# Performance work log

Hardware: AMD Instinct MI355X
Metric: run time of the kernel (lower is better)

## Reference

```python
import jax, jax.numpy as jnp
import numpy as np
from jax.ops import segment_sum


def gcn_conv(x, edge_index, W, b):
    """PyG GCNConv: add self-loops, symmetric D^-1/2 (A+I) D^-1/2 normalization,
    then aggregate normalized messages at target nodes. edge_weight=None -> ones."""
    N = x.shape[0]
    loops = jnp.arange(N, dtype=edge_index.dtype)
    row = jnp.concatenate([edge_index[0], loops])  # source nodes
    col = jnp.concatenate([edge_index[1], loops])  # target nodes
    w = jnp.ones(row.shape[0], dtype=x.dtype)
    deg = segment_sum(w, col, num_segments=N)
    dinv = jnp.where(deg > 0, jax.lax.rsqrt(deg), 0.0)
    norm = dinv[row] * dinv[col]                    # [E+N]
    xw = x @ W                                      # dense transform [N, out]
    msg = xw[row] * norm[:, None]                   # gather + scale [E+N, out]
    out = segment_sum(msg, col, num_segments=N)     # scatter-add at targets
    return out + b


def setup_inputs() -> dict:
    key = jax.random.key(0)
    k1, k2, k3, k4 = jax.random.split(key, 4)
    N, E, nhid, nfeat = 50000, 800000, 256, 128
    x = jax.random.normal(k1, (N, nhid), dtype=jnp.float32)
    edge_index = jax.random.randint(k2, (2, E), 0, N, dtype=jnp.int64)
    W1 = jax.random.normal(k3, (nhid, nhid), dtype=jnp.float32) * (1.0 / np.sqrt(nhid))
    b1 = jnp.zeros((nhid,), dtype=jnp.float32)
    W2 = jax.random.normal(k4, (nhid, nfeat), dtype=jnp.float32) * (1.0 / np.sqrt(nhid))
    b2 = jnp.zeros((nfeat,), dtype=jnp.float32)
    return {"x": x, "edge_index": edge_index, "W1": W1, "b1": b1, "W2": W2, "b2": b2}


def reference(x, edge_index, W1, b1, W2, b2):
    h = jax.nn.relu(gcn_conv(x, edge_index, W1, b1))
    # dropout is identity in eval mode (deterministic reference)
    return gcn_conv(h, edge_index, W2, b2)
```

## Files before the change

### kernel.cpp

```cpp
#include <hip/hip_runtime.h>
#include <math.h>


typedef _Float16 h8 __attribute__((ext_vector_type(8)));
typedef float    f32x4 __attribute__((ext_vector_type(4)));

__global__ void k_init(int* __restrict__ deg, int N,
                       const float* __restrict__ W1, const float* __restrict__ W2,
                       _Float16* __restrict__ wt1, _Float16* __restrict__ wt2,
                       int K, int n1, int n2, int zb)
{
    if ((int)blockIdx.x < zb) {
        int i = blockIdx.x * blockDim.x + threadIdx.x;
        if (i < N) deg[i] = 0;
    } else {
        int i = (blockIdx.x - zb) * blockDim.x + threadIdx.x;
        int c1 = K * n1;
        if (i < c1) {
            int k = i / n1, n = i % n1;
            wt1[(long)n * K + k] = (_Float16)W1[i];
        } else if (i < c1 + K * n2) {
            int j = i - c1;
            int k = j / n2, n = j % n2;
            wt2[(long)n * K + k] = (_Float16)W2[j];
        }
    }
}

__global__ void k_count(const int* __restrict__ col, int E,
                        int* __restrict__ deg, int* __restrict__ rank) {
    int i = blockIdx.x * blockDim.x + threadIdx.x;
    int s = gridDim.x * blockDim.x;
    for (int e = i; e < E; e += s) rank[e] = atomicAdd(&deg[col[e]], 1);
}

__global__ __launch_bounds__(1024) void k_scan1(const int* __restrict__ deg, int N,
                                                int* __restrict__ incl, int* __restrict__ bsum) {
    __shared__ int sm[1024];
    int t = threadIdx.x;
    int i = blockIdx.x * 1024 + t;
    sm[t] = (i < N) ? deg[i] : 0;
    __syncthreads();
    for (int off = 1; off < 1024; off <<= 1) {
        int add = (t >= off) ? sm[t - off] : 0;
        __syncthreads();
        sm[t] += add;
        __syncthreads();
    }
    incl[i] = sm[t];
    if (t == 1023) bsum[blockIdx.x] = sm[t];
}

__global__ void k_scan2(const int* __restrict__ bsum, int* __restrict__ boff, int nb) {
    if (threadIdx.x == 0 && blockIdx.x == 0) {
        int run = 0;
        for (int b = 0; b < nb; b++) { boff[b] = run; run += bsum[b]; }
    }
}

__global__ void k_scan3(const int* __restrict__ incl, const int* __restrict__ boff,
                        const int* __restrict__ deg, int N,
                        int* __restrict__ rowptr, float* __restrict__ dinv) {
    int i = blockIdx.x * blockDim.x + threadIdx.x;
    if (i < N) {
        rowptr[i + 1] = incl[i] + boff[i >> 10];
        dinv[i] = rsqrtf((float)(1 + deg[i]));
    }
    if (i == 0) rowptr[0] = 0;
}

template<bool A32>
__device__ __forceinline__ void gemm_body(
    const float* __restrict__ X32, const _Float16* __restrict__ X16,
    const _Float16* __restrict__ Wt, const float* __restrict__ dinv,
    _Float16* __restrict__ Y, int M, int K, int NC, int bx, int by)
{
    __shared__ _Float16 As[128][40];
    __shared__ _Float16 Bs[128][40];

    const int bn = bx * 128;
    const int bm = by * 128;
    const int tid = threadIdx.x;
    const int w = tid >> 6, l = tid & 63;
    const int wm = (w >> 1) * 64, wn = (w & 1) * 64;
    const int lr = l & 15, lg = l >> 4;

    f32x4 acc[4][4];
    #pragma unroll
    for (int i = 0; i < 4; i++)
        #pragma unroll
        for (int j = 0; j < 4; j++)
            acc[i][j] = (f32x4){0.f, 0.f, 0.f, 0.f};

    for (int k0 = 0; k0 < K; k0 += 32) {
        if (A32) {
            #pragma unroll
            for (int p = 0; p < 2; p++) {
                int rowi = p * 64 + (tid >> 2);
                int colA = (tid & 3) * 8;
                int gm = bm + rowi; if (gm >= M) gm = M - 1;
                float4 f0 = *reinterpret_cast<const float4*>(&X32[(long)gm * K + k0 + colA]);
                float4 f1 = *reinterpret_cast<const float4*>(&X32[(long)gm * K + k0 + colA + 4]);
                h8 hv;
                hv[0] = (_Float16)f0.x; hv[1] = (_Float16)f0.y;
                hv[2] = (_Float16)f0.z; hv[3] = (_Float16)f0.w;
                hv[4] = (_Float16)f1.x; hv[5] = (_Float16)f1.y;
                hv[6] = (_Float16)f1.z; hv[7] = (_Float16)f1.w;
                *reinterpret_cast<h8*>(&As[rowi][colA]) = hv;
            }
        } else {
            int rowi = tid >> 1;
            int colA = (tid & 1) * 16;
            int gm = bm + rowi; if (gm >= M) gm = M - 1;
            *reinterpret_cast<h8*>(&As[rowi][colA]) =
                *reinterpret_cast<const h8*>(&X16[(long)gm * K + k0 + colA]);
            *reinterpret_cast<h8*>(&As[rowi][colA + 8]) =
                *reinterpret_cast<const h8*>(&X16[(long)gm * K + k0 + colA + 8]);
        }
        {
            int n = tid >> 1;
            int colB = (tid & 1) * 16;
            *reinterpret_cast<h8*>(&Bs[n][colB]) =
                *reinterpret_cast<const h8*>(&Wt[(long)(bn + n) * K + k0 + colB]);
            *reinterpret_cast<h8*>(&Bs[n][colB + 8]) =
                *reinterpret_cast<const h8*>(&Wt[(long)(bn + n) * K + k0 + colB + 8]);
        }
        __syncthreads();

        h8 a[4], b[4];
        #pragma unroll
        for (int i = 0; i < 4; i++)
            a[i] = *reinterpret_cast<const h8*>(&As[wm + i * 16 + lr][lg * 8]);
        #pragma unroll
        for (int j = 0; j < 4; j++)
            b[j] = *reinterpret_cast<const h8*>(&Bs[wn + j * 16 + lr][lg * 8]);
        #pragma unroll
        for (int i = 0; i < 4; i++)
            #pragma unroll
            for (int j = 0; j < 4; j++)
                acc[i][j] = __builtin_amdgcn_mfma_f32_16x16x32_f16(
                    a[i], b[j], acc[i][j], 0, 0, 0);
        __syncthreads();
    }

    #pragma unroll
    for (int i = 0; i < 4; i++) {
        #pragma unroll
        for (int r = 0; r < 4; r++) {
            int gm = bm + wm + i * 16 + lg * 4 + r;
            if (gm < M) {
                float s = dinv[gm];
                #pragma unroll
                for (int j = 0; j < 4; j++)
                    Y[(long)gm * NC + bn + wn + j * 16 + lr] =
                        (_Float16)(acc[i][j][r] * s);
            }
        }
    }
}

__global__ __launch_bounds__(256) void k_fill_gemm(
    const int* __restrict__ row, const int* __restrict__ col,
    const int* __restrict__ rank, int E,
    const int* __restrict__ rowptr, int* __restrict__ srcidx,
    int nfb,
    const float* __restrict__ X32, const _Float16* __restrict__ Wt,
    const float* __restrict__ dinv, _Float16* __restrict__ Y,
    int M, int K, int NC, int gx)
{
    if ((int)blockIdx.x < nfb) {
        int i = blockIdx.x * blockDim.x + threadIdx.x;
        int s = nfb * blockDim.x;
        for (int e = i; e < E; e += s) {
            int c = col[e];
            srcidx[rowptr[c] + rank[e]] = row[e];
        }
        return;
    }
    int gb = blockIdx.x - nfb;
    gemm_body<true>(X32, nullptr, Wt, dinv, Y, M, K, NC, gb % gx, gb / gx);
}

__global__ __launch_bounds__(256) void k_gemm16(
    const _Float16* __restrict__ X16, const _Float16* __restrict__ Wt,
    const float* __restrict__ dinv, _Float16* __restrict__ Y,
    int M, int K, int NC)
{
    gemm_body<false>(nullptr, X16, Wt, dinv, Y, M, K, NC, blockIdx.x, blockIdx.y);
}

template<int LPR, bool F16OUT, bool RELU>
__global__ __launch_bounds__(256) void k_agg(
    const int* __restrict__ rowptr, const int* __restrict__ srcidx,
    const _Float16* __restrict__ Y, const float* __restrict__ dinv,
    const float* __restrict__ bias, int N, int FT, int fo,
    float* __restrict__ out32, _Float16* __restrict__ out16)
{
    const int G = 64 / LPR;
    int node = blockIdx.x * 4 + (threadIdx.x >> 6);
    if (node >= N) return;
    int lane = threadIdx.x & 63;
    int sub = lane / LPR;
    int fl  = lane % LPR;
    const int fcol = fo + fl * 8;

    float acc[8];
    if (sub == 0) {
        h8 v = *reinterpret_cast<const h8*>(&Y[(long)node * FT + fcol]);
        #pragma unroll
        for (int j = 0; j < 8; j++) acc[j] = (float)v[j];
    } else {
        #pragma unroll
        for (int j = 0; j < 8; j++) acc[j] = 0.f;
    }

    int beg = rowptr[node], end = rowptr[node + 1];
    int cnt = end - beg;
    int i = beg + sub;
    int full = cnt / (4 * G);
    for (int t = 0; t < full; t++) {
        int r0 = srcidx[i];
        int r1 = srcidx[i + G];
        int r2 = srcidx[i + 2 * G];
        int r3 = srcidx[i + 3 * G];
        h8 v0 = *reinterpret_cast<const h8*>(&Y[(long)r0 * FT + fcol]);
        h8 v1 = *reinterpret_cast<const h8*>(&Y[(long)r1 * FT + fcol]);
        h8 v2 = *reinterpret_cast<const h8*>(&Y[(long)r2 * FT + fcol]);
        h8 v3 = *reinterpret_cast<const h8*>(&Y[(long)r3 * FT + fcol]);
        #pragma unroll
        for (int j = 0; j < 8; j++)
            acc[j] += ((float)v0[j] + (float)v1[j]) + ((float)v2[j] + (float)v3[j]);
        i += 4 * G;
    }
    for (; i < end; i += G) {
        int r = srcidx[i];
        h8 v = *reinterpret_cast<const h8*>(&Y[(long)r * FT + fcol]);
        #pragma unroll
        for (int j = 0; j < 8; j++) acc[j] += (float)v[j];
    }

    #pragma unroll
    for (int m = LPR; m < 64; m <<= 1)
        #pragma unroll
        for (int j = 0; j < 8; j++)
            acc[j] += __shfl_xor(acc[j], m, 64);

    float s = dinv[node];
    const float4* b4 = reinterpret_cast<const float4*>(&bias[fcol]);
    float4 blo = b4[0], bhi = b4[1];
    float r8[8];
    r8[0] = fmaf(s, acc[0], blo.x); r8[1] = fmaf(s, acc[1], blo.y);
    r8[2] = fmaf(s, acc[2], blo.z); r8[3] = fmaf(s, acc[3], blo.w);
    r8[4] = fmaf(s, acc[4], bhi.x); r8[5] = fmaf(s, acc[5], bhi.y);
    r8[6] = fmaf(s, acc[6], bhi.z); r8[7] = fmaf(s, acc[7], bhi.w);
    if (RELU) {
        #pragma unroll
        for (int j = 0; j < 8; j++) r8[j] = fmaxf(r8[j], 0.f);
    }

    long base = (long)node * FT + fcol;
    if (F16OUT) {
        if (sub == 0) {
            h8 o;
            #pragma unroll
            for (int j = 0; j < 8; j++) o[j] = (_Float16)r8[j];
            *reinterpret_cast<h8*>(&out16[base]) = o;
        }
    } else {
        if (sub == 0) {
            *reinterpret_cast<float4*>(&out32[base]) =
                make_float4(r8[0], r8[1], r8[2], r8[3]);
        } else if (sub == 1) {
            *reinterpret_cast<float4*>(&out32[base + 4]) =
                make_float4(r8[4], r8[5], r8[6], r8[7]);
        }
    }
}

extern "C" void kernel_launch(void* const* d_in, const int* in_sizes, int n_in,
                              void* d_out, int out_size, void* d_ws, size_t ws_size,
                              hipStream_t stream)
{
    const float* x   = (const float*)d_in[0];
    const int*   ei  = (const int*)d_in[1];
    const float* W1  = (const float*)d_in[2];
    const float* b1  = (const float*)d_in[3];
    const float* W2  = (const float*)d_in[4];
    const float* b2  = (const float*)d_in[5];

    const int nhid  = in_sizes[3];
    const int nfeat = in_sizes[5];
    const int N     = in_sizes[0] / nhid;
    const int E     = in_sizes[1] / 2;

    const int* row = ei;
    const int* col = ei + E;

    const int nb = (N + 1023) / 1024;

    size_t cur = 0;
    auto alloc = [&](size_t bytes) {
        void* p = (char*)d_ws + cur;
        cur += (bytes + 255) & ~(size_t)255;
        return p;
    };
    float*     dinv   = (float*)alloc((size_t)N * 4);
    int*       deg_i  = (int*)alloc((size_t)N * 4);
    int*       rank   = (int*)alloc((size_t)E * 4);
    int*       rowptr = (int*)alloc((size_t)(N + 1) * 4);
    int*       incl   = (int*)alloc((size_t)nb * 1024 * 4);
    int*       bsum   = (int*)alloc((size_t)nb * 4);
    int*       boff   = (int*)alloc((size_t)nb * 4);
    int*       srcidx = (int*)alloc((size_t)E * 4);
    _Float16*  wt1    = (_Float16*)alloc((size_t)nhid * nhid * 2);
    _Float16*  wt2    = (_Float16*)alloc((size_t)nhid * nfeat * 2);
    _Float16*  y16    = (_Float16*)alloc((size_t)N * nhid * 2);
    _Float16*  h16    = (_Float16*)alloc((size_t)N * nhid * 2);
    _Float16*  y2     = (_Float16*)alloc((size_t)N * nfeat * 2);
    float*     out    = (float*)d_out;
    (void)ws_size; (void)n_in; (void)out_size;

    const int T = 256;

    {
        int zb = (N + T - 1) / T;
        int pb = (nhid * (nhid + nfeat) + T - 1) / T;
        k_init<<<zb + pb, T, 0, stream>>>(deg_i, N, W1, W2, wt1, wt2,
                                          nhid, nhid, nfeat, zb);
    }
    k_count<<<1024, T, 0, stream>>>(col, E, deg_i, rank);
    k_scan1<<<nb, 1024, 0, stream>>>(deg_i, N, incl, bsum);
    k_scan2<<<1, 64, 0, stream>>>(bsum, boff, nb);
    k_scan3<<<(N + T - 1) / T, T, 0, stream>>>(incl, boff, deg_i, N, rowptr, dinv);

    {
        const int nfb = 512;
        int gx = nhid / 128;
        int gy = (N + 127) / 128;
        k_fill_gemm<<<nfb + gx * gy, T, 0, stream>>>(
            row, col, rank, E, rowptr, srcidx, nfb,
            x, wt1, dinv, y16, N, nhid, nhid, gx);
    }

    k_agg<16, true, true><<<(N + 3) / 4, T, 0, stream>>>(
        rowptr, srcidx, y16, dinv, b1, N, nhid, 0, nullptr, h16);
    k_agg<16, true, true><<<(N + 3) / 4, T, 0, stream>>>(
        rowptr, srcidx, y16, dinv, b1, N, nhid, 128, nullptr, h16);

    {
        dim3 grid(nfeat / 128, (N + 127) / 128);
        k_gemm16<<<grid, T, 0, stream>>>(h16, wt2, dinv, y2, N, nhid, nfeat);
    }
    k_agg<16, false, false><<<(N + 3) / 4, T, 0, stream>>>(
        rowptr, srcidx, y2, dinv, b2, N, nfeat, 0, out, nullptr);
}
```

Before: 211.6 us.

## Replace CSR scan with fixed-capacity per-node buckets and overlap counting with GEMM

Drops the three-kernel prefix scan that built rowptr and stores source indices in fixed CAP=64 slots per target node. Edges beyond the cap go to a global overflow list that every aggregation scans. Degree counting now runs alongside the first GEMM, so the GEMM epilogue no longer scales by dinv; the aggregation applies source dinv per edge instead. The GEMM also register-prefetches the next K tile. The cost is a larger srcidx buffer, extra dinv gathers per edge, and a linear overflow scan per node when degrees exceed the cap.

```diff
diff --git a/kernel.cpp b/kernel.cpp
--- a/kernel.cpp
+++ b/kernel.cpp
@@ -5,7 +5,9 @@
 typedef _Float16 h8 __attribute__((ext_vector_type(8)));
 typedef float    f32x4 __attribute__((ext_vector_type(4)));
 
-__global__ void k_init(int* __restrict__ deg, int N,
+#define CAP 64
+
+__global__ void k_init(int* __restrict__ deg, int* __restrict__ govf, int N,
                        const float* __restrict__ W1, const float* __restrict__ W2,
                        _Float16* __restrict__ wt1, _Float16* __restrict__ wt2,
                        int K, int n1, int n2, int zb)
@@ -13,6 +15,7 @@
     if ((int)blockIdx.x < zb) {
         int i = blockIdx.x * blockDim.x + threadIdx.x;
         if (i < N) deg[i] = 0;
+        if (blockIdx.x == 0 && threadIdx.x == 0) *govf = 0;
     } else {
         int i = (blockIdx.x - zb) * blockDim.x + threadIdx.x;
         int c1 = K * n1;
@@ -27,53 +30,11 @@
     }
 }
 
-__global__ void k_count(const int* __restrict__ col, int E,
-                        int* __restrict__ deg, int* __restrict__ rank) {
-    int i = blockIdx.x * blockDim.x + threadIdx.x;
-    int s = gridDim.x * blockDim.x;
-    for (int e = i; e < E; e += s) rank[e] = atomicAdd(&deg[col[e]], 1);
-}
-
-__global__ __launch_bounds__(1024) void k_scan1(const int* __restrict__ deg, int N,
-                                                int* __restrict__ incl, int* __restrict__ bsum) {
-    __shared__ int sm[1024];
-    int t = threadIdx.x;
-    int i = blockIdx.x * 1024 + t;
-    sm[t] = (i < N) ? deg[i] : 0;
-    __syncthreads();
-    for (int off = 1; off < 1024; off <<= 1) {
-        int add = (t >= off) ? sm[t - off] : 0;
-        __syncthreads();
-        sm[t] += add;
-        __syncthreads();
-    }
-    incl[i] = sm[t];
-    if (t == 1023) bsum[blockIdx.x] = sm[t];
-}
-
-__global__ void k_scan2(const int* __restrict__ bsum, int* __restrict__ boff, int nb) {
-    if (threadIdx.x == 0 && blockIdx.x == 0) {
-        int run = 0;
-        for (int b = 0; b < nb; b++) { boff[b] = run; run += bsum[b]; }
-    }
-}
-
-__global__ void k_scan3(const int* __restrict__ incl, const int* __restrict__ boff,
-                        const int* __restrict__ deg, int N,
-                        int* __restrict__ rowptr, float* __restrict__ dinv) {
-    int i = blockIdx.x * blockDim.x + threadIdx.x;
-    if (i < N) {
-        rowptr[i + 1] = incl[i] + boff[i >> 10];
-        dinv[i] = rsqrtf((float)(1 + deg[i]));
-    }
-    if (i == 0) rowptr[0] = 0;
-}
-
 template<bool A32>
 __device__ __forceinline__ void gemm_body(
     const float* __restrict__ X32, const _Float16* __restrict__ X16,
-    const _Float16* __restrict__ Wt, const float* __restrict__ dinv,
-    _Float16* __restrict__ Y, int M, int K, int NC, int bx, int by)
+    const _Float16* __restrict__ Wt, _Float16* __restrict__ Y,
+    int M, int K, int NC, int bx, int by)
 {
     __shared__ _Float16 As[128][40];
     __shared__ _Float16 Bs[128][40];
@@ -85,6 +46,9 @@
     const int wm = (w >> 1) * 64, wn = (w & 1) * 64;
     const int lr = l & 15, lg = l >> 4;
 
+    const int arow = tid >> 2, acol = (tid & 3) * 8;
+    const int xrow = tid >> 1, xcol = (tid & 1) * 16;
+
     f32x4 acc[4][4];
     #pragma unroll
     for (int i = 0; i < 4; i++)
@@ -92,40 +56,52 @@
         for (int j = 0; j < 4; j++)
             acc[i][j] = (f32x4){0.f, 0.f, 0.f, 0.f};
 
+    float4 pf0, pf1, pf2, pf3;
+    h8 pa0, pa1;
+    h8 pb0, pb1;
+
+    auto loadA = [&](int k0) {
+        if (A32) {
+            int gm0 = bm + arow;      if (gm0 >= M) gm0 = M - 1;
+            int gm1 = bm + 64 + arow; if (gm1 >= M) gm1 = M - 1;
+            pf0 = *reinterpret_cast<const float4*>(&X32[(long)gm0 * K + k0 + acol]);
+            pf1 = *reinterpret_cast<const float4*>(&X32[(long)gm0 * K + k0 + acol + 4]);
+            pf2 = *reinterpret_cast<const float4*>(&X32[(long)gm1 * K + k0 + acol]);
+            pf3 = *reinterpret_cast<const float4*>(&X32[(long)gm1 * K + k0 + acol + 4]);
+        } else {
+            int gm = bm + xrow; if (gm >= M) gm = M - 1;
+            pa0 = *reinterpret_cast<const h8*>(&X16[(long)gm * K + k0 + xcol]);
+            pa1 = *reinterpret_cast<const h8*>(&X16[(long)gm * K + k0 + xcol + 8]);
+        }
+    };
+    auto loadB = [&](int k0) {
+        pb0 = *reinterpret_cast<const h8*>(&Wt[(long)(bn + xrow) * K + k0 + xcol]);
+        pb1 = *reinterpret_cast<const h8*>(&Wt[(long)(bn + xrow) * K + k0 + xcol + 8]);
+    };
+
+    loadA(0); loadB(0);
     for (int k0 = 0; k0 < K; k0 += 32) {
         if (A32) {
-            #pragma unroll
-            for (int p = 0; p < 2; p++) {
-                int rowi = p * 64 + (tid >> 2);
-                int colA = (tid & 3) * 8;
-                int gm = bm + rowi; if (gm >= M) gm = M - 1;
-                float4 f0 = *reinterpret_cast<const float4*>(&X32[(long)gm * K + k0 + colA]);
-                float4 f1 = *reinterpret_cast<const float4*>(&X32[(long)gm * K + k0 + colA + 4]);
-                h8 hv;
-                hv[0] = (_Float16)f0.x; hv[1] = (_Float16)f0.y;
-                hv[2] = (_Float16)f0.z; hv[3] = (_Float16)f0.w;
-                hv[4] = (_Float16)f1.x; hv[5] = (_Float16)f1.y;
-                hv[6] = (_Float16)f1.z; hv[7] = (_Float16)f1.w;
-                *reinterpret_cast<h8*>(&As[rowi][colA]) = hv;
-            }
+            h8 h0, h1;
+            h0[0] = (_Float16)pf0.x; h0[1] = (_Float16)pf0.y;
+            h0[2] = (_Float16)pf0.z; h0[3] = (_Float16)pf0.w;
+            h0[4] = (_Float16)pf1.x; h0[5] = (_Float16)pf1.y;
+            h0[6] = (_Float16)pf1.z; h0[7] = (_Float16)pf1.w;
+            h1[0] = (_Float16)pf2.x; h1[1] = (_Float16)pf2.y;
+            h1[2] = (_Float16)pf2.z; h1[3] = (_Float16)pf2.w;
+            h1[4] = (_Float16)pf3.x; h1[5] = (_Float16)pf3.y;
+            h1[6] = (_Float16)pf3.z; h1[7] = (_Float16)pf3.w;
+            *reinterpret_cast<h8*>(&As[arow][acol]) = h0;
+            *reinterpret_cast<h8*>(&As[64 + arow][acol]) = h1;
         } else {
-            int rowi = tid >> 1;
-            int colA = (tid & 1) * 16;
-            int gm = bm + rowi; if (gm >= M) gm = M - 1;
-            *reinterpret_cast<h8*>(&As[rowi][colA]) =
-                *reinterpret_cast<const h8*>(&X16[(long)gm * K + k0 + colA]);
-            *reinterpret_cast<h8*>(&As[rowi][colA + 8]) =
-                *reinterpret_cast<const h8*>(&X16[(long)gm * K + k0 + colA + 8]);
-        }
-        {
-            int n = tid >> 1;
-            int colB = (tid & 1) * 16;
-            *reinterpret_cast<h8*>(&Bs[n][colB]) =
-                *reinterpret_cast<const h8*>(&Wt[(long)(bn + n) * K + k0 + colB]);
-            *reinterpret_cast<h8*>(&Bs[n][colB + 8]) =
-                *reinterpret_cast<const h8*>(&Wt[(long)(bn + n) * K + k0 + colB + 8]);
-        }
+            *reinterpret_cast<h8*>(&As[xrow][xcol]) = pa0;
+            *reinterpret_cast<h8*>(&As[xrow][xcol + 8]) = pa1;
+        }
+        *reinterpret_cast<h8*>(&Bs[xrow][xcol]) = pb0;
+        *reinterpret_cast<h8*>(&Bs[xrow][xcol + 8]) = pb1;
         __syncthreads();
+
+        if (k0 + 32 < K) { loadA(k0 + 32); loadB(k0 + 32); }
 
         h8 a[4], b[4];
         #pragma unroll
@@ -149,51 +125,84 @@
         for (int r = 0; r < 4; r++) {
             int gm = bm + wm + i * 16 + lg * 4 + r;
             if (gm < M) {
-                float s = dinv[gm];
                 #pragma unroll
                 for (int j = 0; j < 4; j++)
                     Y[(long)gm * NC + bn + wn + j * 16 + lr] =
-                        (_Float16)(acc[i][j][r] * s);
+                        (_Float16)acc[i][j][r];
             }
         }
     }
 }
 
-__global__ __launch_bounds__(256) void k_fill_gemm(
+__global__ __launch_bounds__(256) void k_count_gemm(
+    const int* __restrict__ col, int E, int* __restrict__ deg, int* __restrict__ rank,
+    int ncb,
+    const float* __restrict__ X32, const _Float16* __restrict__ Wt,
+    _Float16* __restrict__ Y, int M, int K, int NC, int gx)
+{
+    if ((int)blockIdx.x < ncb) {
+        int i = blockIdx.x * blockDim.x + threadIdx.x;
+        int s = ncb * blockDim.x;
+        for (int e = i; e < E; e += s) rank[e] = atomicAdd(&deg[col[e]], 1);
+        return;
+    }
+    int gb = blockIdx.x - ncb;
+    gemm_body<true>(X32, nullptr, Wt, Y, M, K, NC, gb % gx, gb / gx);
+}
+
+__global__ __launch_bounds__(256) void k_fill_dinv(
     const int* __restrict__ row, const int* __restrict__ col,
     const int* __restrict__ rank, int E,
-    const int* __restrict__ rowptr, int* __restrict__ srcidx,
-    int nfb,
-    const float* __restrict__ X32, const _Float16* __restrict__ Wt,
-    const float* __restrict__ dinv, _Float16* __restrict__ Y,
-    int M, int K, int NC, int gx)
-{
-    if ((int)blockIdx.x < nfb) {
+    const int* __restrict__ deg, float* __restrict__ dinv, int N,
+    int* __restrict__ srcidx, int2* __restrict__ ovf, int* __restrict__ govf,
+    int zb)
+{
+    if ((int)blockIdx.x < zb) {
         int i = blockIdx.x * blockDim.x + threadIdx.x;
-        int s = nfb * blockDim.x;
-        for (int e = i; e < E; e += s) {
-            int c = col[e];
-            srcidx[rowptr[c] + rank[e]] = row[e];
-        }
+        if (i < N) dinv[i] = rsqrtf(1.f + (float)deg[i]);
         return;
     }
-    int gb = blockIdx.x - nfb;
-    gemm_body<true>(X32, nullptr, Wt, dinv, Y, M, K, NC, gb % gx, gb / gx);
+    int g = (blockIdx.x - zb) * blockDim.x + threadIdx.x;
+    int nthreads = (gridDim.x - zb) * blockDim.x;
+    if ((E & 3) == 0) {
+        int G4 = E >> 2;
+        for (int q = g; q < G4; q += nthreads) {
+            int e = q << 2;
+            int4 c4 = *reinterpret_cast<const int4*>(&col[e]);
+            int4 r4 = *reinterpret_cast<const int4*>(&row[e]);
+            int4 k4 = *reinterpret_cast<const int4*>(&rank[e]);
+            if (k4.x < CAP) srcidx[c4.x * CAP + k4.x] = r4.x;
+            else { int o = atomicAdd(govf, 1); ovf[o] = make_int2(r4.x, c4.x); }
+            if (k4.y < CAP) srcidx[c4.y * CAP + k4.y] = r4.y;
+            else { int o = atomicAdd(govf, 1); ovf[o] = make_int2(r4.y, c4.y); }
+            if (k4.z < CAP) srcidx[c4.z * CAP + k4.z] = r4.z;
+            else { int o = atomicAdd(govf, 1); ovf[o] = make_int2(r4.z, c4.z); }
+            if (k4.w < CAP) srcidx[c4.w * CAP + k4.w] = r4.w;
+            else { int o = atomicAdd(govf, 1); ovf[o] = make_int2(r4.w, c4.w); }
+        }
+    } else {
+        for (int e = g; e < E; e += nthreads) {
+            int c = col[e], r = row[e], k = rank[e];
+            if (k < CAP) srcidx[c * CAP + k] = r;
+            else { int o = atomicAdd(govf, 1); ovf[o] = make_int2(r, c); }
+        }
+    }
 }
 
 __global__ __launch_bounds__(256) void k_gemm16(
     const _Float16* __restrict__ X16, const _Float16* __restrict__ Wt,
-    const float* __restrict__ dinv, _Float16* __restrict__ Y,
-    int M, int K, int NC)
-{
-    gemm_body<false>(nullptr, X16, Wt, dinv, Y, M, K, NC, blockIdx.x, blockIdx.y);
+    _Float16* __restrict__ Y, int M, int K, int NC)
+{
+    gemm_body<false>(nullptr, X16, Wt, Y, M, K, NC, blockIdx.x, blockIdx.y);
 }
 
 template<int LPR, bool F16OUT, bool RELU>
 __global__ __launch_bounds__(256) void k_agg(
-    const int* __restrict__ rowptr, const int* __restrict__ srcidx,
-    const _Float16* __restrict__ Y, const float* __restrict__ dinv,
-    const float* __restrict__ bias, int N, int FT, int fo,
+    const int* __restrict__ deg, const float* __restrict__ dinv,
+    const int* __restrict__ srcidx,
+    const int2* __restrict__ ovf, const int* __restrict__ govf,
+    const _Float16* __restrict__ Y, const float* __restrict__ bias,
+    int N, int FT, int fo,
     float* __restrict__ out32, _Float16* __restrict__ out16)
 {
     const int G = 64 / LPR;
@@ -204,39 +213,56 @@
     int fl  = lane % LPR;
     const int fcol = fo + fl * 8;
 
+    float dc = dinv[node];
+    int cnt = min(deg[node], CAP);
+    const int beg = node * CAP;
+
     float acc[8];
     if (sub == 0) {
         h8 v = *reinterpret_cast<const h8*>(&Y[(long)node * FT + fcol]);
         #pragma unroll
-        for (int j = 0; j < 8; j++) acc[j] = (float)v[j];
+        for (int j = 0; j < 8; j++) acc[j] = dc * (float)v[j];
     } else {
         #pragma unroll
         for (int j = 0; j < 8; j++) acc[j] = 0.f;
     }
 
-    int beg = rowptr[node], end = rowptr[node + 1];
-    int cnt = end - beg;
-    int i = beg + sub;
+    int i = sub;
     int full = cnt / (4 * G);
     for (int t = 0; t < full; t++) {
-        int r0 = srcidx[i];
-        int r1 = srcidx[i + G];
-        int r2 = srcidx[i + 2 * G];
-        int r3 = srcidx[i + 3 * G];
+        int r0 = srcidx[beg + i];
+        int r1 = srcidx[beg + i + G];
+        int r2 = srcidx[beg + i + 2 * G];
+        int r3 = srcidx[beg + i + 3 * G];
+        float d0 = dinv[r0], d1 = dinv[r1], d2 = dinv[r2], d3 = dinv[r3];
         h8 v0 = *reinterpret_cast<const h8*>(&Y[(long)r0 * FT + fcol]);
         h8 v1 = *reinterpret_cast<const h8*>(&Y[(long)r1 * FT + fcol]);
         h8 v2 = *reinterpret_cast<const h8*>(&Y[(long)r2 * FT + fcol]);
         h8 v3 = *reinterpret_cast<const h8*>(&Y[(long)r3 * FT + fcol]);
         #pragma unroll
         for (int j = 0; j < 8; j++)
-            acc[j] += ((float)v0[j] + (float)v1[j]) + ((float)v2[j] + (float)v3[j]);
+            acc[j] += (d0 * (float)v0[j] + d1 * (float)v1[j]) +
+                      (d2 * (float)v2[j] + d3 * (float)v3[j]);
         i += 4 * G;
     }
-    for (; i < end; i += G) {
-        int r = srcidx[i];
+    for (; i < cnt; i += G) {
+        int r = srcidx[beg + i];
+        float d = dinv[r];
         h8 v = *reinterpret_cast<const h8*>(&Y[(long)r * FT + fcol]);
         #pragma unroll
-        for (int j = 0; j < 8; j++) acc[j] += (float)v[j];
+        for (int j = 0; j < 8; j++) acc[j] += d * (float)v[j];
+    }
+    {
+        int no = *govf;
+        for (int t = sub; t < no; t += G) {
+            int2 pr = ovf[t];
+            if (pr.y == node) {
+                float d = dinv[pr.x];
+                h8 v = *reinterpret_cast<const h8*>(&Y[(long)pr.x * FT + fcol]);
+                #pragma unroll
+                for (int j = 0; j < 8; j++) acc[j] += d * (float)v[j];
+            }
+        }
     }
 
     #pragma unroll
@@ -245,14 +271,13 @@
         for (int j = 0; j < 8; j++)
             acc[j] += __shfl_xor(acc[j], m, 64);
 
-    float s = dinv[node];
     const float4* b4 = reinterpret_cast<const float4*>(&bias[fcol]);
     float4 blo = b4[0], bhi = b4[1];
     float r8[8];
-    r8[0] = fmaf(s, acc[0], blo.x); r8[1] = fmaf(s, acc[1], blo.y);
-    r8[2] = fmaf(s, acc[2], blo.z); r8[3] = fmaf(s, acc[3], blo.w);
-    r8[4] = fmaf(s, acc[4], bhi.x); r8[5] = fmaf(s, acc[5], bhi.y);
-    r8[6] = fmaf(s, acc[6], bhi.z); r8[7] = fmaf(s, acc[7], bhi.w);
+    r8[0] = fmaf(dc, acc[0], blo.x); r8[1] = fmaf(dc, acc[1], blo.y);
+    r8[2] = fmaf(dc, acc[2], blo.z); r8[3] = fmaf(dc, acc[3], blo.w);
+    r8[4] = fmaf(dc, acc[4], bhi.x); r8[5] = fmaf(dc, acc[5], bhi.y);
+    r8[6] = fmaf(dc, acc[6], bhi.z); r8[7] = fmaf(dc, acc[7], bhi.w);
     if (RELU) {
         #pragma unroll
         for (int j = 0; j < 8; j++) r8[j] = fmaxf(r8[j], 0.f);
@@ -295,8 +320,6 @@
 
     const int* row = ei;
     const int* col = ei + E;
-
-    const int nb = (N + 1023) / 1024;
 
     size_t cur = 0;
     auto alloc = [&](size_t bytes) {
@@ -307,11 +330,9 @@
     float*     dinv   = (float*)alloc((size_t)N * 4);
     int*       deg_i  = (int*)alloc((size_t)N * 4);
     int*       rank   = (int*)alloc((size_t)E * 4);
-    int*       rowptr = (int*)alloc((size_t)(N + 1) * 4);
-    int*       incl   = (int*)alloc((size_t)nb * 1024 * 4);
-    int*       bsum   = (int*)alloc((size_t)nb * 4);
-    int*       boff   = (int*)alloc((size_t)nb * 4);
-    int*       srcidx = (int*)alloc((size_t)E * 4);
+    int*       srcidx = (int*)alloc((size_t)N * CAP * 4);
+    int2*      ovf    = (int2*)alloc((size_t)E * 8);
+    int*       govf   = (int*)alloc(256);
     _Float16*  wt1    = (_Float16*)alloc((size_t)nhid * nhid * 2);
     _Float16*  wt2    = (_Float16*)alloc((size_t)nhid * nfeat * 2);
     _Float16*  y16    = (_Float16*)alloc((size_t)N * nhid * 2);
@@ -321,36 +342,34 @@
     (void)ws_size; (void)n_in; (void)out_size;
 
     const int T = 256;
+    const int zb = (N + T - 1) / T;
 
     {
-        int zb = (N + T - 1) / T;
         int pb = (nhid * (nhid + nfeat) + T - 1) / T;
-        k_init<<<zb + pb, T, 0, stream>>>(deg_i, N, W1, W2, wt1, wt2,
+        k_init<<<zb + pb, T, 0, stream>>>(deg_i, govf, N, W1, W2, wt1, wt2,
                                           nhid, nhid, nfeat, zb);
     }
-    k_count<<<1024, T, 0, stream>>>(col, E, deg_i, rank);
-    k_scan1<<<nb, 1024, 0, stream>>>(deg_i, N, incl, bsum);
-    k_scan2<<<1, 64, 0, stream>>>(bsum, boff, nb);
-    k_scan3<<<(N + T - 1) / T, T, 0, stream>>>(incl, boff, deg_i, N, rowptr, dinv);
 
     {
-        const int nfb = 512;
+        const int ncb = 256;
         int gx = nhid / 128;
         int gy = (N + 127) / 128;
-        k_fill_gemm<<<nfb + gx * gy, T, 0, stream>>>(
-            row, col, rank, E, rowptr, srcidx, nfb,
-            x, wt1, dinv, y16, N, nhid, nhid, gx);
-    }
+        k_count_gemm<<<ncb + gx * gy, T, 0, stream>>>(
+            col, E, deg_i, rank, ncb, x, wt1, y16, N, nhid, nhid, gx);
+    }
+
+    k_fill_dinv<<<zb + 1024, T, 0, stream>>>(
+        row, col, rank, E, deg_i, dinv, N, srcidx, ovf, govf, zb);
 
     k_agg<16, true, true><<<(N + 3) / 4, T, 0, stream>>>(
-        rowptr, srcidx, y16, dinv, b1, N, nhid, 0, nullptr, h16);
+        deg_i, dinv, srcidx, ovf, govf, y16, b1, N, nhid, 0, nullptr, h16);
     k_agg<16, true, true><<<(N + 3) / 4, T, 0, stream>>>(
-        rowptr, srcidx, y16, dinv, b1, N, nhid, 128, nullptr, h16);
+        deg_i, dinv, srcidx, ovf, govf, y16, b1, N, nhid, 128, nullptr, h16);
 
     {
         dim3 grid(nfeat / 128, (N + 127) / 128);
-        k_gemm16<<<grid, T, 0, stream>>>(h16, wt2, dinv, y2, N, nhid, nfeat);
+        k_gemm16<<<grid, T, 0, stream>>>(h16, wt2, y2, N, nhid, nfeat);
     }
     k_agg<16, false, false><<<(N + 3) / 4, T, 0, stream>>>(
-        rowptr, srcidx, y2, dinv, b2, N, nfeat, 0, out, nullptr);
-}
+        deg_i, dinv, srcidx, ovf, govf, y2, b2, N, nfeat, 0, out, nullptr);
+}
```

After: 180.5 us. 1.17x faster.
